# Optimization experiments

Hardware: AMD Instinct MI355X
Metric: run time of the kernel (lower is better)

Reference implementation:

```python
import jax, jax.numpy as jnp
import numpy as np

S = 7  # output_size


def _bin_indices(lo, hi, dim):
    """PyTorch AdaptiveMaxPool windows for each of S bins over [lo, hi] (inclusive).
    Returns gather indices [R,S,K] and validity mask [R,S,K].
    start_i = floor(i*L/S), end_i = ceil((i+1)*L/S), L = hi-lo+1."""
    L = hi - lo + 1  # [R]
    i = jnp.arange(S)
    start = lo[:, None] + (i * L[:, None]) // S          # [R,S]
    end = lo[:, None] + ((i + 1) * L[:, None] + S - 1) // S  # [R,S]
    K = (dim + S - 1) // S + 1  # static max window size
    k = jnp.arange(K)
    idx = start[:, :, None] + k                          # [R,S,K]
    valid = idx < end[:, :, None]
    return jnp.clip(idx, 0, dim - 1), valid


def setup_inputs() -> dict:
    key = jax.random.key(0)
    k1, k2 = jax.random.split(key)
    feature_map = jax.random.normal(k1, (1, 256, 64, 64), dtype=jnp.float32)
    # generate valid ROIs: sort coordinate pairs so x1<=x2, y1<=y2
    pairs = jax.random.randint(k2, (1, 128, 2, 2), 0, 64)  # [B,R,(x|y),2]
    pairs = jnp.sort(pairs, axis=-1)
    rois = jnp.stack(
        [pairs[..., 0, 0], pairs[..., 1, 0], pairs[..., 0, 1], pairs[..., 1, 1]],
        axis=-1,
    ).astype(jnp.int32)  # [1,128,4] = (x1,y1,x2,y2)
    return {"feature_map": feature_map, "rois": rois}


def reference(feature_map, rois):
    f = feature_map[0]  # [C,H,W]  (module only works with batch=1)
    C, H, W = f.shape
    r = rois.reshape(-1, 4).astype(jnp.int32)
    x1, y1, x2, y2 = r[:, 0], r[:, 1], r[:, 2], r[:, 3]
    neg = jnp.finfo(f.dtype).min

    # pool over dim 2 (x / f_wid axis, per original slicing feature_map[:,:,x1:x2+1,...])
    h_idx, h_val = _bin_indices(x1, x2, H)               # [R,S,Kh]
    g1 = f[:, h_idx, :]                                  # [C,R,S,Kh,W]
    rowmax = jnp.max(jnp.where(h_val[None, :, :, :, None], g1, neg), axis=3)  # [C,R,S,W]

    # pool over dim 3 (y / f_hei axis)
    w_idx, w_val = _bin_indices(y1, y2, W)               # [R,S,Kw]
    R_, Sw, Kw = w_idx.shape
    g2 = jnp.take_along_axis(rowmax, w_idx.reshape(1, R_, 1, Sw * Kw), axis=3)
    g2 = g2.reshape(C, R_, S, Sw, Kw)                    # [C,R,S,S,Kw]
    pooled = jnp.max(jnp.where(w_val[None, :, None, :, :], g2, neg), axis=4)  # [C,R,S,S]

    # pooled_rois[b, roi, c, S, S] -> flatten to [1, R, C, S*S]
    out = pooled.transpose(1, 0, 2, 3).reshape(1, R_, C, S * S)
    return out
```

## Files before the change

kernel.cpp:

```cpp
#include <hip/hip_runtime.h>

#define NS 7
#define NC 256
#define NH 64
#define NW 64
#define NR 128

__global__ __launch_bounds__(256) void roi_pool_kernel(
    const float* __restrict__ f,
    const int* __restrict__ rois,
    float* __restrict__ out,
    int total)
{
    int t = blockIdx.x * blockDim.x + threadIdx.x;
    if (t >= total) return;

    int bin = t % (NS * NS);
    int tc  = t / (NS * NS);
    int c   = tc % NC;
    int r   = tc / NC;
    int i   = bin / NS;
    int j   = bin % NS;

    int x1 = rois[4 * r + 0];
    int y1 = rois[4 * r + 1];
    int x2 = rois[4 * r + 2];
    int y2 = rois[4 * r + 3];

    int Lh = x2 - x1 + 1;
    int Lw = y2 - y1 + 1;

    int rs = x1 + (i * Lh) / NS;
    int re = x1 + ((i + 1) * Lh + NS - 1) / NS;
    int cs = y1 + (j * Lw) / NS;
    int ce = y1 + ((j + 1) * Lw + NS - 1) / NS;

    const float* fc = f + (size_t)c * (NH * NW);

    float m = -3.402823466e+38f;
    for (int h = rs; h < re; ++h) {
        const float* row = fc + h * NW;
        for (int w = cs; w < ce; ++w) {
            m = fmaxf(m, row[w]);
        }
    }

    out[t] = m;
}

extern "C" void kernel_launch(void* const* d_in, const int* in_sizes, int n_in,
                              void* d_out, int out_size, void* d_ws, size_t ws_size,
                              hipStream_t stream)
{
    const float* feature_map = (const float*)d_in[0];
    const int*   rois        = (const int*)d_in[1];
    float*       out         = (float*)d_out;

    int total = NR * NC * NS * NS;
    int block = 256;
    int grid  = (total + block - 1) / block;

    roi_pool_kernel<<<grid, block, 0, stream>>>(feature_map, rois, out, total);
}
```

Baseline: 27.39 us.

## Separate ROI max pooling into column-max pass and LDS bin reduction

Each wavefront now handles one (roi, channel) pair. Lanes map to ROI columns and take the max over each bin's rows with coalesced loads, storing the column maxima in LDS. After a barrier, 49 lanes reduce those column maxima into the 7x7 bins. This replaces the old per-bin scalar loops that reread overlapping windows with uncoalesced accesses. In exchange it adds a block-wide barrier, and when the ROI is narrow many lanes sit idle.

```diff
diff --git a/kernel.cpp b/kernel.cpp
--- a/kernel.cpp
+++ b/kernel.cpp
@@ -1,4 +1,5 @@
 #include <hip/hip_runtime.h>
+#include <cfloat>
 
 #define NS 7
 #define NC 256
@@ -9,43 +10,53 @@
 __global__ __launch_bounds__(256) void roi_pool_kernel(
     const float* __restrict__ f,
     const int* __restrict__ rois,
-    float* __restrict__ out,
-    int total)
+    float* __restrict__ out)
 {
-    int t = blockIdx.x * blockDim.x + threadIdx.x;
-    if (t >= total) return;
+    __shared__ float colmax_lds[4][NS][NW];
 
-    int bin = t % (NS * NS);
-    int tc  = t / (NS * NS);
-    int c   = tc % NC;
-    int r   = tc / NC;
-    int i   = bin / NS;
-    int j   = bin % NS;
+    const int lane = threadIdx.x & 63;
+    const int wid  = threadIdx.x >> 6;
 
-    int x1 = rois[4 * r + 0];
-    int y1 = rois[4 * r + 1];
-    int x2 = rois[4 * r + 2];
-    int y2 = rois[4 * r + 3];
+    const int r  = blockIdx.x >> 6;
+    const int cg = blockIdx.x & 63;
+    const int c  = cg * 4 + wid;
 
-    int Lh = x2 - x1 + 1;
-    int Lw = y2 - y1 + 1;
-
-    int rs = x1 + (i * Lh) / NS;
-    int re = x1 + ((i + 1) * Lh + NS - 1) / NS;
-    int cs = y1 + (j * Lw) / NS;
-    int ce = y1 + ((j + 1) * Lw + NS - 1) / NS;
+    const int x1 = rois[4 * r + 0];
+    const int y1 = rois[4 * r + 1];
+    const int x2 = rois[4 * r + 2];
+    const int y2 = rois[4 * r + 3];
+    const int Lh = x2 - x1 + 1;
+    const int Lw = y2 - y1 + 1;
 
     const float* fc = f + (size_t)c * (NH * NW);
 
-    float m = -3.402823466e+38f;
-    for (int h = rs; h < re; ++h) {
-        const float* row = fc + h * NW;
-        for (int w = cs; w < ce; ++w) {
-            m = fmaxf(m, row[w]);
+    for (int i = 0; i < NS; ++i) {
+        const int hs = x1 + (i * Lh) / NS;
+        const int he = x1 + ((i + 1) * Lh + NS - 1) / NS;
+        float m = -FLT_MAX;
+        if (lane < Lw) {
+            const float* p = fc + hs * NW + y1 + lane;
+            for (int h = hs; h < he; ++h) {
+                m = fmaxf(m, *p);
+                p += NW;
+            }
         }
+        colmax_lds[wid][i][lane] = m;
     }
 
-    out[t] = m;
+    __syncthreads();
+
+    if (lane < NS * NS) {
+        const int i  = lane / NS;
+        const int j  = lane % NS;
+        const int cs = (j * Lw) / NS;
+        const int ce = ((j + 1) * Lw + NS - 1) / NS;
+        float m = -FLT_MAX;
+        #pragma unroll 1
+        for (int k = cs; k < ce; ++k)
+            m = fmaxf(m, colmax_lds[wid][i][k]);
+        out[((size_t)(r * NC + c)) * (NS * NS) + lane] = m;
+    }
 }
 
 extern "C" void kernel_launch(void* const* d_in, const int* in_sizes, int n_in,
@@ -56,9 +67,8 @@
     const int*   rois        = (const int*)d_in[1];
     float*       out         = (float*)d_out;
 
-    int total = NR * NC * NS * NS;
-    int block = 256;
-    int grid  = (total + block - 1) / block;
+    const int grid  = NR * (NC / 4);
+    const int block = 256;
 
-    roi_pool_kernel<<<grid, block, 0, stream>>>(feature_map, rois, out, total);
+    roi_pool_kernel<<<grid, block, 0, stream>>>(feature_map, rois, out);
 }
```

Result: slower. 28.01 us (+2.3%).
